# Kernel tuning notes

Measured on AMD Instinct MI355X. Metric: run time of the kernel, lower is better.

The kernel has to match this reference:

```python
import jax
import jax.numpy as jnp
import numpy as np

VOCAB = 16384
WIDTH = 256
BETA = 0.25
EPS = 1e-12  # F.normalize eps


def setup_inputs() -> dict:
    key = jax.random.key(0)
    k1, k2, k3 = jax.random.split(key, 3)
    class_tokens = jax.random.normal(k1, (32, 1, WIDTH), dtype=jnp.float32)
    patch_tokens = jax.random.normal(k2, (32, WIDTH, 16, 16), dtype=jnp.float32)
    W = jax.random.normal(k3, (VOCAB, WIDTH), dtype=jnp.float32) * 0.02  # codebook
    return {"class_tokens": class_tokens, "patch_tokens": patch_tokens, "W": W}


def _l2norm(x):
    return x / jnp.maximum(jnp.linalg.norm(x, axis=-1, keepdims=True), EPS)


def reference(class_tokens, patch_tokens, W):
    B, L, C = class_tokens.shape
    _, _, H, Wd = patch_tokens.shape
    # (B,C,H,W) -> (B,HW,C)
    pt = patch_tokens.reshape(B, C, H * Wd).transpose(0, 2, 1)
    NxC = jnp.concatenate([class_tokens, pt], axis=1).reshape(-1, C)  # [N,C]

    # vocab_norm branch: cosine-similarity argmax on detached, normalized vectors
    xn = _l2norm(jax.lax.stop_gradient(NxC))      # [N,C]
    Wn = _l2norm(W)                                # [V,C] (column-normalized W.T)
    sim = xn @ Wn.T                                # [N,V] big matmul
    idx = jnp.argmax(sim, axis=1)                  # [N]

    counts = jnp.zeros((VOCAB,), jnp.float32).at[idx].add(1.0)  # bincount

    fhat_g = W[idx]                                # codebook gather [N,C]
    vq_loss = BETA * jnp.mean((jax.lax.stop_gradient(fhat_g) - NxC) ** 2) \
              + jnp.mean((fhat_g - jax.lax.stop_gradient(NxC)) ** 2)

    # straight-through estimator
    fhat = jax.lax.stop_gradient(fhat_g - NxC) + NxC

    prob = counts / counts.sum()
    vocab_usage = jnp.mean((prob > 0.01 / VOCAB).astype(jnp.float32)) * 100.0

    fhat = fhat.reshape(B, L + H * Wd, C)
    fhat_class = fhat[:, :L, :]
    fhat_patch = fhat[:, L:, :].reshape(B, H, Wd, C).transpose(0, 3, 1, 2)
    return fhat_class, fhat_patch, vq_loss, vocab_usage
```

## Files before the change

kernel.cpp:

```cpp
#include <hip/hip_runtime.h>
#include <stdint.h>

#define VOCAB 16384
#define NB 32
#define NTOK 8224
#define MTILES 65
#define MP 8320
#define NBY 128
#define TILE_BYTES 65536
#define PHASE_BYTES 16384
#define NLOSS 2056
#define MWIN 2.2e-3f

typedef _Float16 half8 __attribute__((ext_vector_type(8)));
typedef float f4 __attribute__((ext_vector_type(4)));
typedef __attribute__((address_space(1))) const uint32_t* gas_t;
typedef __attribute__((address_space(3))) uint32_t* las_t;

__device__ __forceinline__ void async16(const void* g, void* l) {
    __builtin_amdgcn_global_load_lds((gas_t)g, (las_t)l, 16, 0, 0);
}

__device__ __forceinline__ unsigned long long key64(float v, int idx) {
    unsigned u = __float_as_uint(v);
    u = (u & 0x80000000u) ? ~u : (u | 0x80000000u);
    return ((unsigned long long)u << 32) | (unsigned)(~idx);
}

__device__ __forceinline__ float keyval(unsigned long long k) {
    unsigned u = (unsigned)(k >> 32);
    u = (u & 0x80000000u) ? (u & 0x7fffffffu) : ~u;
    return __uint_as_float(u);
}

__device__ __forceinline__ void merge2(unsigned long long& k1, unsigned long long& k2,
                                       unsigned long long p1, unsigned long long p2) {
    unsigned long long lo = k1 < p1 ? k1 : p1;
    k1 = k1 > p1 ? k1 : p1;
    unsigned long long m2 = k2 > p2 ? k2 : p2;
    k2 = lo > m2 ? lo : m2;
}

__global__ __launch_bounds__(256) void k_class(const float* __restrict__ cls, float* __restrict__ tok) {
    int b = blockIdx.x, c = threadIdx.x;
    tok[(b * 257) * 256 + c] = cls[b * 256 + c];
}

__global__ __launch_bounds__(256) void k_patch(const float* __restrict__ patch, float* __restrict__ tok) {
    __shared__ float t[64][65];
    int c0 = blockIdx.x * 64, p0 = blockIdx.y * 64, b = blockIdx.z;
    int tid = threadIdx.x;
    int l = tid & 63, w = tid >> 6;
    const float* src = patch + b * 65536;
#pragma unroll
    for (int i = 0; i < 16; ++i) {
        int row = i * 4 + w;
        t[row][l] = src[(c0 + row) * 256 + p0 + l];
    }
    __syncthreads();
#pragma unroll
    for (int i = 0; i < 16; ++i) {
        int prow = i * 4 + w;
        tok[(b * 257 + 1 + p0 + prow) * 256 + c0 + l] = t[l][prow];
    }
}

__global__ __launch_bounds__(256) void k_pack(const float* __restrict__ src, char* __restrict__ dst,
                                              float* __restrict__ norms, int nrows) {
    __shared__ float t[16][264];
    __shared__ float pr[16][16];
    __shared__ float sn[16];
    int g = blockIdx.x;
    int row0 = g * 16;
    int tid = threadIdx.x;
    int rr = tid >> 4, cb = tid & 15;
    int grow = row0 + rr;
    const float* sp = src + (size_t)grow * 256 + cb * 16;
    float psum = 0.0f;
#pragma unroll
    for (int i = 0; i < 4; ++i) {
        float4 v = (grow < nrows) ? *(const float4*)(sp + i * 4) : make_float4(0.f, 0.f, 0.f, 0.f);
        *(float4*)&t[rr][cb * 16 + i * 4] = v;
        psum += v.x * v.x + v.y * v.y + v.z * v.z + v.w * v.w;
    }
    pr[rr][cb] = psum;
    __syncthreads();
    if (tid < 16) {
        float s = 0.0f;
#pragma unroll
        for (int j = 0; j < 16; ++j) s += pr[tid][j];
        float nv = fmaxf(sqrtf(s), 1e-12f);
        sn[tid] = nv;
        norms[row0 + tid] = nv;
    }
    __syncthreads();
    int c = tid & 63, pair = tid >> 6;
    int m = c & 15, jb = (c >> 4) * 8;
    float inv = 1.0f / sn[m];
    char* base = dst + (size_t)(g >> 3) * TILE_BYTES + (size_t)(g & 7) * 1024 + c * 16;
#pragma unroll
    for (int it = 0; it < 2; ++it) {
        int k32 = it * 4 + pair;
        const float* rowp = &t[m][k32 * 32 + jb];
        half8 o;
#pragma unroll
        for (int j = 0; j < 8; ++j) o[j] = (_Float16)(rowp[j] * inv);
        *(half8*)(base + (size_t)k32 * 8192) = o;
    }
}

__global__ __launch_bounds__(256) void k_sim(const char* __restrict__ apk, const char* __restrict__ bpk,
                                             unsigned long long* __restrict__ pb) {
    __shared__ char lds[32768];
    int id = blockIdx.x;
    int xcd = id & 7, r = id >> 3;
    int st = r / 104, within = r % 104;
    int stid = xcd * 10 + st;
    int sx = stid % 5, sy = stid / 5;
    int bx = sx * 13 + within % 13;
    int by = sy * 8 + within / 13;

    int tid = threadIdx.x;
    int ln = tid & 63, wv = tid >> 6;
    int mh = wv >> 1, nh = wv & 1;
    const char* abase = apk + (size_t)bx * TILE_BYTES;
    const char* bbase = bpk + (size_t)by * TILE_BYTES;

    f4 acc[4][4];
#pragma unroll
    for (int i = 0; i < 4; ++i)
#pragma unroll
        for (int j = 0; j < 4; ++j) acc[i][j] = (f4){0.f, 0.f, 0.f, 0.f};

#pragma unroll
    for (int i = 0; i < 8; ++i) {
        int c = wv * 8 + i;
        const char* g = (c < 16 ? abase + (c << 10) : bbase + ((c - 16) << 10)) + (ln << 4);
        async16(g, lds + (c << 10));
    }

    for (int p = 0; p < 4; ++p) {
        __syncthreads();
        half8 ah[2][4], bh[2][4];
#pragma unroll
        for (int s = 0; s < 2; ++s) {
            const half8* Af = (const half8*)(lds + s * 8192);
            const half8* Bf = (const half8*)(lds + 16384 + s * 8192);
#pragma unroll
            for (int mi = 0; mi < 4; ++mi) ah[s][mi] = Af[(mh * 4 + mi) * 64 + ln];
#pragma unroll
            for (int ni = 0; ni < 4; ++ni) bh[s][ni] = Bf[(nh * 4 + ni) * 64 + ln];
        }
        __syncthreads();
        if (p < 3) {
            const char* a2 = abase + (p + 1) * PHASE_BYTES;
            const char* b2 = bbase + (p + 1) * PHASE_BYTES;
#pragma unroll
            for (int i = 0; i < 8; ++i) {
                int c = wv * 8 + i;
                const char* g = (c < 16 ? a2 + (c << 10) : b2 + ((c - 16) << 10)) + (ln << 4);
                async16(g, lds + (c << 10));
            }
        }
#pragma unroll
        for (int s = 0; s < 2; ++s)
#pragma unroll
            for (int mi = 0; mi < 4; ++mi)
#pragma unroll
                for (int ni = 0; ni < 4; ++ni)
                    acc[mi][ni] = __builtin_amdgcn_mfma_f32_16x16x32_f16(bh[s][ni], ah[s][mi], acc[mi][ni], 0, 0, 0);
    }

    int col = ln & 15, quad = ln >> 4;
    unsigned long long* s1 = (unsigned long long*)lds;
    unsigned long long* s2 = (unsigned long long*)(lds + 2048);
    __syncthreads();
    int nbase = by * 128 + nh * 64 + quad * 4;
#pragma unroll
    for (int mi = 0; mi < 4; ++mi) {
        float v1 = -2.0f, v2 = -2.5f;
        int j1 = 0, j2 = 0;
#pragma unroll
        for (int ni = 0; ni < 4; ++ni)
#pragma unroll
            for (int rg = 0; rg < 4; ++rg) {
                float v = acc[mi][ni][rg];
                int sid = ni * 16 + rg;
                bool g1 = v > v1;
                bool g2 = v > v2;
                v2 = g1 ? v1 : (g2 ? v : v2);
                j2 = g1 ? j1 : (g2 ? sid : j2);
                v1 = g1 ? v : v1;
                j1 = g1 ? sid : j1;
            }
        unsigned long long k1 = key64(v1, nbase + j1);
        unsigned long long k2 = key64(v2, nbase + j2);
#pragma unroll
        for (int off = 16; off < 64; off <<= 1) {
            unsigned long long p1 = __shfl_xor(k1, off);
            unsigned long long p2 = __shfl_xor(k2, off);
            merge2(k1, k2, p1, p2);
        }
        if (quad == 0) {
            int row = mh * 64 + mi * 16 + col;
            s1[row * 2 + nh] = k1;
            s2[row * 2 + nh] = k2;
        }
    }
    __syncthreads();
    if (tid < 128) {
        unsigned long long k1 = s1[tid * 2], k2 = s2[tid * 2];
        merge2(k1, k2, s1[tid * 2 + 1], s2[tid * 2 + 1]);
        ulonglong2 v; v.x = k1; v.y = k2;
        ((ulonglong2*)pb)[((size_t)bx * 128 + tid) * 128 + by] = v;
    }
}

__global__ __launch_bounds__(256) void k_gather(const unsigned long long* __restrict__ pb,
                                                const float* __restrict__ W, const float* __restrict__ tok,
                                                const float* __restrict__ ntok, const float* __restrict__ nw,
                                                float* __restrict__ out, int* __restrict__ idxbuf,
                                                float* __restrict__ lossbuf, unsigned int* __restrict__ used) {
    __shared__ float lp[4];
    int tid = threadIdx.x;
    int t = blockIdx.x * 4 + (tid >> 6);
    int ln = tid & 63, w = tid >> 6;
    const ulonglong2* pv = (const ulonglong2*)pb;
    ulonglong2 ea = pv[(size_t)t * 128 + ln];
    ulonglong2 eb = pv[(size_t)t * 128 + 64 + ln];
    unsigned long long g = ea.x > eb.x ? ea.x : eb.x;
#pragma unroll
    for (int off = 1; off < 64; off <<= 1) {
        unsigned long long o = __shfl_xor(g, off);
        if (o > g) g = o;
    }
    float T = keyval(g) - MWIN;
    f4 xv = *(const f4*)&tok[(size_t)t * 256 + ln * 4];
    float nt = ntok[t];
    unsigned long long k4[4] = {ea.x, ea.y, eb.x, eb.y};
    float bestv = -3.0f;
    int besti = 0x7fffffff;
#pragma unroll
    for (int gi = 0; gi < 4; ++gi) {
        unsigned long long mask = __ballot(keyval(k4[gi]) >= T);
        while (mask) {
            int src = __ffsll((unsigned long long)mask) - 1;
            mask &= mask - 1;
            unsigned long long ck = __shfl(k4[gi], src);
            int ci = (int)(~(unsigned)(ck & 0xffffffffu));
            f4 wc = *(const f4*)&W[(size_t)ci * 256 + ln * 4];
            float d = xv.x * wc.x + xv.y * wc.y + xv.z * wc.z + xv.w * wc.w;
#pragma unroll
            for (int off = 1; off < 64; off <<= 1) d += __shfl_xor(d, off);
            float sim = d / (nt * nw[ci]);
            if (sim > bestv || (sim == bestv && ci < besti)) { bestv = sim; besti = ci; }
        }
    }
    int bi = besti;
    f4 wr = *(const f4*)&W[(size_t)bi * 256 + ln * 4];
    float dx = wr.x - xv.x, dy = wr.y - xv.y, dz = wr.z - xv.z, dw = wr.w - xv.w;
    float ls = dx * dx + dy * dy + dz * dz + dw * dw;
#pragma unroll
    for (int off = 1; off < 64; off <<= 1) ls += __shfl_xor(ls, off);
    if (ln == 0) {
        lp[w] = ls;
        atomicOr(&used[bi >> 5], 1u << (bi & 31));
        idxbuf[t] = bi;
    }
    if (t % 257 == 0) {
        int b = t / 257;
        *(f4*)&out[b * 256 + ln * 4] = wr;
    }
    __syncthreads();
    if (tid == 0) lossbuf[blockIdx.x] = lp[0] + lp[1] + lp[2] + lp[3];
}

__global__ __launch_bounds__(256) void k_scatter(const int* __restrict__ idxbuf, const float* __restrict__ W,
                                                 float* __restrict__ out) {
    __shared__ float t64[64][65];
    __shared__ int sidx[64];
    int c0 = blockIdx.x * 64, p0 = blockIdx.y * 64, b = blockIdx.z;
    int tid = threadIdx.x;
    if (tid < 64) sidx[tid] = idxbuf[b * 257 + 1 + p0 + tid];
    __syncthreads();
    int l = tid & 63, w = tid >> 6;
#pragma unroll
    for (int i = 0; i < 16; ++i) {
        int p = i * 4 + w;
        t64[p][l] = W[(size_t)sidx[p] * 256 + c0 + l];
    }
    __syncthreads();
#pragma unroll
    for (int i = 0; i < 16; ++i) {
        int c = i * 4 + w;
        out[8192 + (size_t)b * 65536 + (size_t)(c0 + c) * 256 + p0 + l] = t64[l][c];
    }
}

__global__ __launch_bounds__(256) void k_final(const unsigned int* __restrict__ used,
                                               const float* __restrict__ lossbuf, float* __restrict__ out) {
    int tid = threadIdx.x;
    int cnt = 0;
    float ls = 0.0f;
    for (int i = tid; i < VOCAB / 32; i += 256) cnt += __popc(used[i]);
    for (int i = tid; i < NLOSS; i += 256) ls += lossbuf[i];
#pragma unroll
    for (int off = 32; off > 0; off >>= 1) {
        cnt += __shfl_down(cnt, off);
        ls += __shfl_down(ls, off);
    }
    __shared__ int p4[4];
    __shared__ float f4s[4];
    if ((tid & 63) == 0) { p4[tid >> 6] = cnt; f4s[tid >> 6] = ls; }
    __syncthreads();
    if (tid == 0) {
        int c = p4[0] + p4[1] + p4[2] + p4[3];
        float l = f4s[0] + f4s[1] + f4s[2] + f4s[3];
        out[8192 + 2097152] = 1.25f * l / (float)(NTOK * 256);
        out[8192 + 2097152 + 1] = 100.0f * (float)c / (float)VOCAB;
    }
}

extern "C" void kernel_launch(void* const* d_in, const int* in_sizes, int n_in,
                              void* d_out, int out_size, void* d_ws, size_t ws_size,
                              hipStream_t stream) {
    (void)in_sizes; (void)n_in; (void)out_size; (void)ws_size;
    const float* cls = (const float*)d_in[0];
    const float* patch = (const float*)d_in[1];
    const float* W = (const float*)d_in[2];
    float* out = (float*)d_out;

    char* ws = (char*)d_ws;
    float* tok = (float*)ws;
    char* apk = ws + (size_t)NTOK * 256 * 4;
    char* bpk = apk + (size_t)MTILES * TILE_BYTES;
    unsigned long long* pb = (unsigned long long*)(bpk + (size_t)NBY * TILE_BYTES);
    float* ntokv = (float*)(pb + (size_t)MP * NBY * 2);
    float* nwv = ntokv + MP;
    float* lossbuf = nwv + VOCAB;
    int* idxbuf = (int*)(lossbuf + NLOSS);
    unsigned int* used = (unsigned int*)(idxbuf + NTOK);

    hipMemsetAsync(used, 0, (VOCAB / 32) * sizeof(unsigned int), stream);

    k_class<<<NB, 256, 0, stream>>>(cls, tok);
    k_patch<<<dim3(4, 4, NB), 256, 0, stream>>>(patch, tok);
    k_pack<<<MTILES * 8, 256, 0, stream>>>(tok, apk, ntokv, NTOK);
    k_pack<<<VOCAB / 16, 256, 0, stream>>>(W, bpk, nwv, VOCAB);
    k_sim<<<MTILES * NBY, 256, 0, stream>>>(apk, bpk, pb);
    k_gather<<<NLOSS, 256, 0, stream>>>(pb, W, tok, ntokv, nwv, out, idxbuf, lossbuf, used);
    k_scatter<<<dim3(4, 4, NB), 256, 0, stream>>>(idxbuf, W, out);
    k_final<<<1, 256, 0, stream>>>(used, lossbuf, out);
}
```

Measured before the change: 211.7 us.

## Merge small kernels into fewer launches and pack index into sim value low bits

Removes the class-token copy kernel by having the pack and gather kernels read class tokens directly, merges the two pack launches into one grid, and folds the final reduction into block 0 of the scatter kernel. In the similarity epilogue, the top-2 tracking now embeds a 4-bit local index into the low mantissa bits of each value so plain fmin/fmax can replace the compare-and-select chains. This cuts launch count and epilogue ALU work but perturbs similarity values slightly, which the gather rescoring window (widened a bit) must absorb. Folding the final reduction into scatter block 0 looks unsafe: that block may read used/lossbuf correctly since gather has finished, but it runs alongside other scatter blocks, which is fine here.

```diff
diff --git a/kernel.cpp b/kernel.cpp
--- a/kernel.cpp
+++ b/kernel.cpp
@@ -10,7 +10,8 @@
 #define TILE_BYTES 65536
 #define PHASE_BYTES 16384
 #define NLOSS 2056
-#define MWIN 2.2e-3f
+#define MWIN 2.25e-3f
+#define TOKCHUNKS 520
 
 typedef _Float16 half8 __attribute__((ext_vector_type(8)));
 typedef float f4 __attribute__((ext_vector_type(4)));
@@ -41,11 +42,6 @@
     k2 = lo > m2 ? lo : m2;
 }
 
-__global__ __launch_bounds__(256) void k_class(const float* __restrict__ cls, float* __restrict__ tok) {
-    int b = blockIdx.x, c = threadIdx.x;
-    tok[(b * 257) * 256 + c] = cls[b * 256 + c];
-}
-
 __global__ __launch_bounds__(256) void k_patch(const float* __restrict__ patch, float* __restrict__ tok) {
     __shared__ float t[64][65];
     int c0 = blockIdx.x * 64, p0 = blockIdx.y * 64, b = blockIdx.z;
@@ -65,17 +61,30 @@
     }
 }
 
-__global__ __launch_bounds__(256) void k_pack(const float* __restrict__ src, char* __restrict__ dst,
-                                              float* __restrict__ norms, int nrows) {
+__global__ __launch_bounds__(256) void k_pack2(const float* __restrict__ tok, const float* __restrict__ cls,
+                                               const float* __restrict__ W, char* __restrict__ apk,
+                                               char* __restrict__ bpk, float* __restrict__ ntokv,
+                                               float* __restrict__ nwv) {
     __shared__ float t[16][264];
     __shared__ float pr[16][16];
     __shared__ float sn[16];
-    int g = blockIdx.x;
+    int g0 = blockIdx.x;
+    bool isTok = g0 < TOKCHUNKS;
+    int g = isTok ? g0 : g0 - TOKCHUNKS;
+    char* dst = isTok ? apk : bpk;
+    float* norms = isTok ? ntokv : nwv;
+    int nrows = isTok ? NTOK : VOCAB;
     int row0 = g * 16;
     int tid = threadIdx.x;
     int rr = tid >> 4, cb = tid & 15;
     int grow = row0 + rr;
-    const float* sp = src + (size_t)grow * 256 + cb * 16;
+    const float* sp;
+    if (isTok) {
+        int b = grow / 257, s = grow - b * 257;
+        sp = (s == 0) ? (cls + (size_t)b * 256 + cb * 16) : (tok + (size_t)grow * 256 + cb * 16);
+    } else {
+        sp = W + (size_t)grow * 256 + cb * 16;
+    }
     float psum = 0.0f;
 #pragma unroll
     for (int i = 0; i < 4; ++i) {
@@ -178,23 +187,23 @@
     int nbase = by * 128 + nh * 64 + quad * 4;
 #pragma unroll
     for (int mi = 0; mi < 4; ++mi) {
-        float v1 = -2.0f, v2 = -2.5f;
-        int j1 = 0, j2 = 0;
+        float v1 = -3.0f, v2 = -3.5f;
 #pragma unroll
         for (int ni = 0; ni < 4; ++ni)
 #pragma unroll
             for (int rg = 0; rg < 4; ++rg) {
-                float v = acc[mi][ni][rg];
-                int sid = ni * 16 + rg;
-                bool g1 = v > v1;
-                bool g2 = v > v2;
-                v2 = g1 ? v1 : (g2 ? v : v2);
-                j2 = g1 ? j1 : (g2 ? sid : j2);
-                v1 = g1 ? v : v1;
-                j1 = g1 ? sid : j1;
+                unsigned e = 15u - (unsigned)(ni * 4 + rg);
+                float pv = __uint_as_float((__float_as_uint(acc[mi][ni][rg]) & 0xFFFFFFF0u) | e);
+                float tmn = fminf(v1, pv);
+                v1 = fmaxf(v1, pv);
+                v2 = fmaxf(v2, tmn);
             }
-        unsigned long long k1 = key64(v1, nbase + j1);
-        unsigned long long k2 = key64(v2, nbase + j2);
+        int o1 = 15 - (int)(__float_as_uint(v1) & 15u);
+        int o2 = 15 - (int)(__float_as_uint(v2) & 15u);
+        int n1 = ((o1 >> 2) << 4) | (o1 & 3);
+        int n2 = ((o2 >> 2) << 4) | (o2 & 3);
+        unsigned long long k1 = key64(v1, nbase + n1);
+        unsigned long long k2 = key64(v2, nbase + n2);
 #pragma unroll
         for (int off = 16; off < 64; off <<= 1) {
             unsigned long long p1 = __shfl_xor(k1, off);
@@ -218,6 +227,7 @@
 
 __global__ __launch_bounds__(256) void k_gather(const unsigned long long* __restrict__ pb,
                                                 const float* __restrict__ W, const float* __restrict__ tok,
+                                                const float* __restrict__ cls,
                                                 const float* __restrict__ ntok, const float* __restrict__ nw,
                                                 float* __restrict__ out, int* __restrict__ idxbuf,
                                                 float* __restrict__ lossbuf, unsigned int* __restrict__ used) {
@@ -235,7 +245,9 @@
         if (o > g) g = o;
     }
     float T = keyval(g) - MWIN;
-    f4 xv = *(const f4*)&tok[(size_t)t * 256 + ln * 4];
+    int tq = t / 257, ts = t - tq * 257;
+    const float* xrow = (ts == 0) ? (cls + (size_t)tq * 256) : (tok + (size_t)t * 256);
+    f4 xv = *(const f4*)&xrow[ln * 4];
     float nt = ntok[t];
     unsigned long long k4[4] = {ea.x, ea.y, eb.x, eb.y};
     float bestv = -3.0f;
@@ -267,16 +279,16 @@
         atomicOr(&used[bi >> 5], 1u << (bi & 31));
         idxbuf[t] = bi;
     }
-    if (t % 257 == 0) {
-        int b = t / 257;
-        *(f4*)&out[b * 256 + ln * 4] = wr;
+    if (ts == 0) {
+        *(f4*)&out[tq * 256 + ln * 4] = wr;
     }
     __syncthreads();
     if (tid == 0) lossbuf[blockIdx.x] = lp[0] + lp[1] + lp[2] + lp[3];
 }
 
 __global__ __launch_bounds__(256) void k_scatter(const int* __restrict__ idxbuf, const float* __restrict__ W,
-                                                 float* __restrict__ out) {
+                                                 float* __restrict__ out, const unsigned int* __restrict__ used,
+                                                 const float* __restrict__ lossbuf) {
     __shared__ float t64[64][65];
     __shared__ int sidx[64];
     int c0 = blockIdx.x * 64, p0 = blockIdx.y * 64, b = blockIdx.z;
@@ -295,29 +307,26 @@
         int c = i * 4 + w;
         out[8192 + (size_t)b * 65536 + (size_t)(c0 + c) * 256 + p0 + l] = t64[l][c];
     }
-}
-
-__global__ __launch_bounds__(256) void k_final(const unsigned int* __restrict__ used,
-                                               const float* __restrict__ lossbuf, float* __restrict__ out) {
-    int tid = threadIdx.x;
-    int cnt = 0;
-    float ls = 0.0f;
-    for (int i = tid; i < VOCAB / 32; i += 256) cnt += __popc(used[i]);
-    for (int i = tid; i < NLOSS; i += 256) ls += lossbuf[i];
-#pragma unroll
-    for (int off = 32; off > 0; off >>= 1) {
-        cnt += __shfl_down(cnt, off);
-        ls += __shfl_down(ls, off);
-    }
-    __shared__ int p4[4];
-    __shared__ float f4s[4];
-    if ((tid & 63) == 0) { p4[tid >> 6] = cnt; f4s[tid >> 6] = ls; }
-    __syncthreads();
-    if (tid == 0) {
-        int c = p4[0] + p4[1] + p4[2] + p4[3];
-        float l = f4s[0] + f4s[1] + f4s[2] + f4s[3];
-        out[8192 + 2097152] = 1.25f * l / (float)(NTOK * 256);
-        out[8192 + 2097152 + 1] = 100.0f * (float)c / (float)VOCAB;
+    if (blockIdx.x == 0 && blockIdx.y == 0 && blockIdx.z == 0) {
+        int cnt = 0;
+        float ls = 0.0f;
+        for (int i = tid; i < VOCAB / 32; i += 256) cnt += __popc(used[i]);
+        for (int i = tid; i < NLOSS; i += 256) ls += lossbuf[i];
+#pragma unroll
+        for (int off = 32; off > 0; off >>= 1) {
+            cnt += __shfl_down(cnt, off);
+            ls += __shfl_down(ls, off);
+        }
+        __shared__ int p4f[4];
+        __shared__ float f4s[4];
+        if ((tid & 63) == 0) { p4f[tid >> 6] = cnt; f4s[tid >> 6] = ls; }
+        __syncthreads();
+        if (tid == 0) {
+            int c = p4f[0] + p4f[1] + p4f[2] + p4f[3];
+            float lsum = f4s[0] + f4s[1] + f4s[2] + f4s[3];
+            out[8192 + 2097152] = 1.25f * lsum / (float)(NTOK * 256);
+            out[8192 + 2097152 + 1] = 100.0f * (float)c / (float)VOCAB;
+        }
     }
 }
 
@@ -343,12 +352,9 @@
 
     hipMemsetAsync(used, 0, (VOCAB / 32) * sizeof(unsigned int), stream);
 
-    k_class<<<NB, 256, 0, stream>>>(cls, tok);
     k_patch<<<dim3(4, 4, NB), 256, 0, stream>>>(patch, tok);
-    k_pack<<<MTILES * 8, 256, 0, stream>>>(tok, apk, ntokv, NTOK);
-    k_pack<<<VOCAB / 16, 256, 0, stream>>>(W, bpk, nwv, VOCAB);
+    k_pack2<<<TOKCHUNKS + VOCAB / 16, 256, 0, stream>>>(tok, cls, W, apk, bpk, ntokv, nwv);
     k_sim<<<MTILES * NBY, 256, 0, stream>>>(apk, bpk, pb);
-    k_gather<<<NLOSS, 256, 0, stream>>>(pb, W, tok, ntokv, nwv, out, idxbuf, lossbuf, used);
-    k_scatter<<<dim3(4, 4, NB), 256, 0, stream>>>(idxbuf, W, out);
-    k_final<<<1, 256, 0, stream>>>(used, lossbuf, out);
-}
+    k_gather<<<NLOSS, 256, 0, stream>>>(pb, W, tok, cls, ntokv, nwv, out, idxbuf, lossbuf, used);
+    k_scatter<<<dim3(4, 4, NB), 256, 0, stream>>>(idxbuf, W, out, used, lossbuf);
+}
```

Result: faster. 203.2 us (-4.0%).
